# Kernel tuning notes

Hardware: AMD Instinct MI355X
Metric: run time of the kernel (lower is better)

The kernel has to match this reference:

```python
import jax, jax.numpy as jnp
import numpy as np

HEADS = 16
DIM_HEAD = 64
SCALE = 8.0
NUM_NULL_KV = 2
NON_CAUSAL_PREFIX = 64
LN_EPS = 1e-5

def _l2norm(t):
    # F.normalize: t / max(||t||_2, eps)
    n = jnp.sqrt(jnp.sum(t * t, axis=-1, keepdims=True))
    return t / jnp.maximum(n, 1e-12)

def _layer_norm(x, gamma):
    mu = jnp.mean(x, axis=-1, keepdims=True)
    var = jnp.mean((x - mu) ** 2, axis=-1, keepdims=True)
    return (x - mu) * jax.lax.rsqrt(var + LN_EPS) * gamma  # beta buffer is zeros

def setup_inputs() -> dict:
    key = jax.random.key(0)
    ks = jax.random.split(key, 6)
    b, n, dim = 2, 2048, 1024
    inner = HEADS * DIM_HEAD
    return {
        "x": jax.random.normal(ks[0], (b, n, dim), jnp.float32),
        "gamma": jnp.ones((dim,), jnp.float32),
        "Wq": jax.random.normal(ks[1], (dim, inner), jnp.float32) * (dim ** -0.5),
        "Wkv": jax.random.normal(ks[2], (dim, 2 * DIM_HEAD), jnp.float32) * (dim ** -0.5),
        "q_scale": jnp.ones((DIM_HEAD,), jnp.float32),
        "k_scale": jnp.ones((DIM_HEAD,), jnp.float32),
        "null_kv": jax.random.normal(ks[3], (2, NUM_NULL_KV, DIM_HEAD), jnp.float32),
        "Wout": jax.random.normal(ks[4], (inner, dim), jnp.float32) * (inner ** -0.5),
    }

def reference(x, gamma, Wq, Wkv, q_scale, k_scale, null_kv, Wout):
    b, n, dim = x.shape
    # NOTE: in the torch module, kv_input = x BEFORE self.norm is applied
    kv = jnp.einsum('bnd,de->bne', x, Wkv)          # [b, n, 2*dh]
    k, v = kv[..., :DIM_HEAD], kv[..., DIM_HEAD:]    # single shared kv head (MQA)
    xn = _layer_norm(x, gamma)
    q = jnp.einsum('bnd,de->bne', xn, Wq)            # [b, n, h*dh]
    # null kv prepended
    null_k = jnp.broadcast_to(null_kv[0], (b, NUM_NULL_KV, DIM_HEAD))
    null_v = jnp.broadcast_to(null_kv[1], (b, NUM_NULL_KV, DIM_HEAD))
    k = jnp.concatenate([null_k, k], axis=1)         # [b, j, dh]
    v = jnp.concatenate([null_v, v], axis=1)
    q = q.reshape(b, n, HEADS, DIM_HEAD).transpose(0, 2, 1, 3)  # [b, h, n, dh]
    q = _l2norm(q) * q_scale
    k = _l2norm(k) * k_scale
    sim = jnp.einsum('bhid,bjd->bhij', q, k) * SCALE  # [b, h, i, j]
    i, j = n, k.shape[1]
    rows = jnp.arange(i)[:, None]
    cols = jnp.arange(j)[None, :]
    causal_mask = cols > rows + (j - i)               # triu(j - i + 1)
    prefix_free = (rows < NON_CAUSAL_PREFIX) & (cols < NON_CAUSAL_PREFIX + (j - i))
    causal_mask = causal_mask & (~prefix_free)
    neg = -jnp.finfo(sim.dtype).max
    sim = jnp.where(causal_mask, neg, sim)
    attn = jax.nn.softmax(sim, axis=-1)
    out = jnp.einsum('bhij,bjd->bhid', attn, v)       # [b, h, n, dh]
    out = out.transpose(0, 2, 1, 3).reshape(b, n, HEADS * DIM_HEAD)
    return jnp.einsum('bne,ed->bnd', out, Wout)
```

## Files before the change

kernel.cpp:

```cpp
#include <hip/hip_runtime.h>

typedef _Float16 h16;
typedef _Float16 f16x8 __attribute__((ext_vector_type(8)));
typedef _Float16 f16x4 __attribute__((ext_vector_type(4)));
typedef float f32x4 __attribute__((ext_vector_type(4)));

#define KSCALE_FOLD 11.541560327111707f

__global__ __launch_bounds__(256) void pre_k(const float* __restrict__ Wq,
    const float* __restrict__ Wkv, const float* __restrict__ Wout,
    const float* __restrict__ gamma, const float* __restrict__ x,
    const float* __restrict__ nkv, const float* __restrict__ kscale,
    h16* __restrict__ W1t, h16* __restrict__ Wot, float* __restrict__ cq,
    float* __restrict__ mu, float* __restrict__ rr, h16* __restrict__ xh,
    h16* __restrict__ Kh, h16* __restrict__ Vth)
{
    __shared__ float ts[64][65];
    int pid = blockIdx.x;
    int tid = threadIdx.x;
    if (pid < 544) {
        int bx = pid & 15, by = pid >> 4;
        int c = tid & 63, rc = tid >> 6;
        const float* src; int ld, scol, drow0; h16* dst; bool useg = false;
        if (by < 16)      { src = Wq;   ld = 1024; scol = by*64;       dst = W1t; drow0 = scol;        useg = true; }
        else if (by < 18) { src = Wkv;  ld = 128;  scol = (by-16)*64;  dst = W1t; drow0 = 1024 + scol; }
        else              { src = Wout; ld = 1024; scol = (by-18)*64;  dst = Wot; drow0 = scol; }
        float part = 0.f;
#pragma unroll
        for (int i = 0; i < 16; ++i) {
            int r = rc*16 + i;
            float v = src[(size_t)(bx*64 + r)*ld + scol + c];
            if (useg) v *= gamma[bx*64 + r];
            part += v;
            ts[r][c] = v;
        }
        if (useg) atomicAdd(&cq[scol + c], part);
        __syncthreads();
#pragma unroll
        for (int i = 0; i < 16; ++i) {
            int r = rc*16 + i;
            dst[(size_t)(drow0 + r)*1024 + bx*64 + c] = (h16)ts[c][r];
        }
    } else if (pid < 1568) {
        int w = tid >> 6, l = tid & 63;
        int row = (pid - 544)*4 + w;
        const float* xr = x + (size_t)row*1024;
        float s = 0.f, ss = 0.f;
        float4 v[4];
#pragma unroll
        for (int i = 0; i < 4; ++i) {
            v[i] = *(const float4*)(xr + i*256 + l*4);
            s  += v[i].x + v[i].y + v[i].z + v[i].w;
            ss += v[i].x*v[i].x + v[i].y*v[i].y + v[i].z*v[i].z + v[i].w*v[i].w;
        }
#pragma unroll
        for (int m = 1; m < 64; m <<= 1) { s += __shfl_xor(s, m); ss += __shfl_xor(ss, m); }
        float m_ = s * (1.f/1024.f);
        float var = ss * (1.f/1024.f) - m_*m_;
        float r_ = rsqrtf(var + 1e-5f);
        if (l == 0) { mu[row] = m_; rr[row] = r_; }
        h16* xo = xh + (size_t)row*1024;
#pragma unroll
        for (int i = 0; i < 4; ++i) {
            f16x4 hv = { (h16)v[i].x, (h16)v[i].y, (h16)v[i].z, (h16)v[i].w };
            *(f16x4*)(xo + i*256 + l*4) = hv;
        }
    } else {
        int nb = pid - 1568;
        if (nb == 0 && tid < 128) {
            int t = tid >> 6, d = tid & 63;
            float kv = nkv[(0*2 + t)*64 + d];
            float ss = kv*kv;
#pragma unroll
            for (int m = 1; m < 64; m <<= 1) ss += __shfl_xor(ss, m);
            float inv = 1.f / fmaxf(sqrtf(ss), 1e-12f);
            h16 kvh = (h16)(kv * inv * kscale[d] * KSCALE_FOLD);
            Kh[(size_t)(0*2112 + t)*64 + d] = kvh;
            Kh[(size_t)(1*2112 + t)*64 + d] = kvh;
            float nv = nkv[(2 + t)*64 + d];
            Vth[(size_t)(0*64 + d)*2112 + t] = (h16)nv;
            Vth[(size_t)(1*64 + d)*2112 + t] = (h16)nv;
        }
        for (int idx = nb*256 + tid; idx < 2*62*64; idx += 2048) {
            int b = idx / (62*64), rem = idx % (62*64);
            int j = 2050 + rem/64, d = rem & 63;
            Kh[((size_t)b*2112 + j)*64 + d] = (h16)0.f;
            Vth[((size_t)b*64 + d)*2112 + j] = (h16)0.f;
        }
    }
}

template<int MODE>
__global__ __launch_bounds__(256) void gemm_k(
    const h16* __restrict__ A, const h16* __restrict__ B,
    const float* __restrict__ mu, const float* __restrict__ rr, const float* __restrict__ cq,
    const float* __restrict__ qscale, const float* __restrict__ kscale,
    h16* __restrict__ Qh, h16* __restrict__ Kh, h16* __restrict__ Vth, float* __restrict__ outp)
{
    __shared__ h16 As[2][128*64];
    __shared__ h16 Bs[2][64*64];
    int tid = threadIdx.x;
    int w = tid >> 6, l = tid & 63;
    int lq = l & 15, qq = l >> 4;
    int arow0 = blockIdx.y*128, bcol0 = blockIdx.x*64;
    const int K = 1024;
    f32x4 acc[2][4] = {};

    auto STAGE = [&](int buf, int kt) {
#pragma unroll
        for (int i = 0; i < 4; ++i) {
            int s = i*256 + tid;
            int row = s >> 3;
            int cb = ((s & 7)*16) ^ ((row & 7) << 4);
            const char* asrc = (const char*)(A + (size_t)(arow0 + row)*K + kt) + cb;
            __builtin_amdgcn_global_load_lds(
                (const __attribute__((address_space(1))) unsigned int*)asrc,
                (__attribute__((address_space(3))) unsigned int*)((char*)&As[buf][0] + s*16), 16, 0, 0);
        }
#pragma unroll
        for (int i = 0; i < 2; ++i) {
            int s = i*256 + tid;
            int row = s >> 3;
            int cb = ((s & 7)*16) ^ ((row & 7) << 4);
            const char* bsrc = (const char*)(B + (size_t)(bcol0 + row)*K + kt) + cb;
            __builtin_amdgcn_global_load_lds(
                (const __attribute__((address_space(1))) unsigned int*)bsrc,
                (__attribute__((address_space(3))) unsigned int*)((char*)&Bs[buf][0] + s*16), 16, 0, 0);
        }
    };

    STAGE(0, 0);
    int cur = 0;
    for (int kt = 0; kt < K; kt += 64) {
        int nkt = (kt + 64 < K) ? kt + 64 : kt;
        STAGE(cur ^ 1, nkt);
        asm volatile("s_waitcnt vmcnt(6)" ::: "memory");
        __builtin_amdgcn_s_barrier();
        __builtin_amdgcn_sched_barrier(0);
        const char* Ab = (const char*)&As[cur][0];
        const char* Bb = (const char*)&Bs[cur][0];
#pragma unroll
        for (int kc = 0; kc < 2; ++kc) {
            int cb = (kc*64 + qq*16) ^ ((lq & 7) << 4);
            f16x8 af[2], bf[4];
#pragma unroll
            for (int mt = 0; mt < 2; ++mt)
                af[mt] = *(const f16x8*)(Ab + (w*32 + mt*16 + lq)*128 + cb);
#pragma unroll
            for (int nt = 0; nt < 4; ++nt)
                bf[nt] = *(const f16x8*)(Bb + (nt*16 + lq)*128 + cb);
#pragma unroll
            for (int mt = 0; mt < 2; ++mt)
#pragma unroll
                for (int nt = 0; nt < 4; ++nt)
                    acc[mt][nt] = __builtin_amdgcn_mfma_f32_16x16x32_f16(af[mt], bf[nt], acc[mt][nt], 0, 0, 0);
        }
        __builtin_amdgcn_sched_barrier(0);
        __builtin_amdgcn_s_barrier();
        cur ^= 1;
    }
    asm volatile("s_waitcnt vmcnt(0)" ::: "memory");

    int wrow0 = arow0 + w*32;
    int bx = blockIdx.x;
    if (MODE == 1) {
#pragma unroll
        for (int mt = 0; mt < 2; ++mt)
#pragma unroll
            for (int nt = 0; nt < 4; ++nt)
#pragma unroll
                for (int i = 0; i < 4; ++i)
                    outp[(size_t)(wrow0 + mt*16 + qq*4 + i)*1024 + bcol0 + nt*16 + lq] = acc[mt][nt][i];
        return;
    }
    if (bx < 16) {
        float cqv[4], qs[4];
#pragma unroll
        for (int nt = 0; nt < 4; ++nt) {
            cqv[nt] = cq[bcol0 + nt*16 + lq];
            qs[nt] = qscale[nt*16 + lq];
        }
#pragma unroll
        for (int mt = 0; mt < 2; ++mt) {
            float muv[4], rv[4], ssq[4], qv[4][4];
#pragma unroll
            for (int i = 0; i < 4; ++i) {
                int row = wrow0 + mt*16 + qq*4 + i;
                muv[i] = mu[row]; rv[i] = rr[row]; ssq[i] = 0.f;
            }
#pragma unroll
            for (int nt = 0; nt < 4; ++nt)
#pragma unroll
                for (int i = 0; i < 4; ++i) {
                    float q = rv[i]*(acc[mt][nt][i] - muv[i]*cqv[nt]);
                    qv[nt][i] = q; ssq[i] += q*q;
                }
#pragma unroll
            for (int i = 0; i < 4; ++i) {
                float s2 = ssq[i];
                s2 += __shfl_xor(s2, 1); s2 += __shfl_xor(s2, 2);
                s2 += __shfl_xor(s2, 4); s2 += __shfl_xor(s2, 8);
                ssq[i] = 1.f / fmaxf(sqrtf(s2), 1e-12f);
            }
#pragma unroll
            for (int nt = 0; nt < 4; ++nt)
#pragma unroll
                for (int i = 0; i < 4; ++i) {
                    int row = wrow0 + mt*16 + qq*4 + i;
                    Qh[(size_t)row*1024 + bcol0 + nt*16 + lq] = (h16)(qv[nt][i]*ssq[i]*qs[nt]);
                }
        }
    } else if (bx == 16) {
        float ks[4];
#pragma unroll
        for (int nt = 0; nt < 4; ++nt) ks[nt] = kscale[nt*16 + lq] * KSCALE_FOLD;
#pragma unroll
        for (int mt = 0; mt < 2; ++mt) {
            float ssq[4] = {0.f, 0.f, 0.f, 0.f};
#pragma unroll
            for (int nt = 0; nt < 4; ++nt)
#pragma unroll
                for (int i = 0; i < 4; ++i) ssq[i] += acc[mt][nt][i]*acc[mt][nt][i];
#pragma unroll
            for (int i = 0; i < 4; ++i) {
                float s2 = ssq[i];
                s2 += __shfl_xor(s2, 1); s2 += __shfl_xor(s2, 2);
                s2 += __shfl_xor(s2, 4); s2 += __shfl_xor(s2, 8);
                ssq[i] = 1.f / fmaxf(sqrtf(s2), 1e-12f);
            }
#pragma unroll
            for (int nt = 0; nt < 4; ++nt)
#pragma unroll
                for (int i = 0; i < 4; ++i) {
                    int row = wrow0 + mt*16 + qq*4 + i;
                    int b = row >> 11, ii = row & 2047;
                    Kh[((size_t)b*2112 + 2 + ii)*64 + nt*16 + lq] = (h16)(acc[mt][nt][i]*ssq[i]*ks[nt]);
                }
        }
    } else {
#pragma unroll
        for (int mt = 0; mt < 2; ++mt)
#pragma unroll
            for (int nt = 0; nt < 4; ++nt)
#pragma unroll
                for (int i = 0; i < 4; ++i) {
                    int row = wrow0 + mt*16 + qq*4 + i;
                    int b = row >> 11, ii = row & 2047;
                    Vth[((size_t)b*64 + nt*16 + lq)*2112 + 2 + ii] = (h16)acc[mt][nt][i];
                }
    }
}

__global__ __launch_bounds__(512, 4) void attn_k(const h16* __restrict__ Qh,
    const h16* __restrict__ Kh, const h16* __restrict__ Vth, h16* __restrict__ Oh)
{
    __shared__ h16 KVs[2][2][64*64];
    __shared__ h16 Ps[8][16*64];
    int id = blockIdx.x;
    int hp = id & 7;
    int b = (id >> 3) & 1;
    int u = id >> 4;
    int qt = (u < 16) ? u : 47 - u;
    int tid = threadIdx.x, w = tid >> 6, l = tid & 63;
    int h = hp*2 + (w >> 2);
    int wq = w & 3;
    int lq = l & 15, qq = l >> 4;
    int qstart = qt * 64;
    int q0w = qstart + wq * 16;
    h16* P = &Ps[w][0];
    int xs = (lq & 7) << 4;

    f16x8 qf[2];
#pragma unroll
    for (int kc = 0; kc < 2; ++kc)
        qf[kc] = *(const f16x8*)(Qh + (size_t)(b*2048 + q0w + lq)*1024 + h*64 + kc*32 + qq*8);

    int qrow = q0w + lq;
    int thr = (qrow < 64) ? 65 : qrow + 2;

    int srow = tid >> 3;
    int cbs = ((tid & 7)*16) ^ ((srow & 7) << 4);
    const char* ksrc = (const char*)(Kh + (size_t)b*2112*64) + (size_t)srow*128 + cbs;
    const char* vsrc = (const char*)(Vth + (size_t)b*64*2112) + (size_t)srow*4224 + cbs;

    f32x4 oacc[4] = {};
    float lrun = 0.f;

    int lastc = qstart + 65;
    int ntile = lastc/64 + 1;

    auto STAGE = [&](int buf, int kv0) {
        __builtin_amdgcn_global_load_lds(
            (const __attribute__((address_space(1))) unsigned int*)(ksrc + (size_t)kv0*128),
            (__attribute__((address_space(3))) unsigned int*)((char*)&KVs[buf][0][0] + tid*16), 16, 0, 0);
        __builtin_amdgcn_global_load_lds(
            (const __attribute__((address_space(1))) unsigned int*)(vsrc + (size_t)kv0*2),
            (__attribute__((address_space(3))) unsigned int*)((char*)&KVs[buf][1][0] + tid*16), 16, 0, 0);
    };

    STAGE(0, 0);
    int cur = 0;
    for (int t = 0; t < ntile; ++t) {
        int kv0 = t*64;
        int nxt = (t + 1 < ntile) ? t + 1 : t;
        STAGE(cur ^ 1, nxt*64);
        asm volatile("s_waitcnt vmcnt(2)" ::: "memory");
        __builtin_amdgcn_s_barrier();
        __builtin_amdgcn_sched_barrier(0);

        bool active = (kv0 <= q0w + 17) || (q0w < 64 && kv0 < 66);
        if (active) {
            const char* Kl = (const char*)&KVs[cur][0][0];
            const char* Vl = (const char*)&KVs[cur][1][0];
            f32x4 s[4] = {};
#pragma unroll
            for (int kc = 0; kc < 2; ++kc) {
                int ko = (kc*64 + qq*16) ^ xs;
                f16x8 kf[4];
#pragma unroll
                for (int mt = 0; mt < 4; ++mt)
                    kf[mt] = *(const f16x8*)(Kl + (mt*16 + lq)*128 + ko);
#pragma unroll
                for (int mt = 0; mt < 4; ++mt)
                    s[mt] = __builtin_amdgcn_mfma_f32_16x16x32_f16(kf[mt], qf[kc], s[mt], 0, 0, 0);
            }
            if (kv0 + 63 > q0w + 2) {
#pragma unroll
                for (int mt = 0; mt < 4; ++mt)
#pragma unroll
                    for (int i = 0; i < 4; ++i) {
                        int kv = kv0 + mt*16 + qq*4 + i;
                        if (kv > thr) s[mt][i] = -__builtin_inff();
                    }
            }
            float ps = 0.f;
#pragma unroll
            for (int mt = 0; mt < 4; ++mt)
#pragma unroll
                for (int i = 0; i < 4; ++i) {
                    float p = exp2f(s[mt][i]);
                    s[mt][i] = p; ps += p;
                }
            ps += __shfl_xor(ps, 16);
            ps += __shfl_xor(ps, 32);
            lrun += ps;
#pragma unroll
            for (int mt = 0; mt < 4; ++mt) {
                uint2 pk;
                pk.x = __builtin_bit_cast(unsigned int, __builtin_amdgcn_cvt_pkrtz(s[mt][0], s[mt][1]));
                pk.y = __builtin_bit_cast(unsigned int, __builtin_amdgcn_cvt_pkrtz(s[mt][2], s[mt][3]));
                *(uint2*)((char*)P + lq*128 + ((mt*32 + qq*8) ^ xs)) = pk;
            }
#pragma unroll
            for (int kc = 0; kc < 2; ++kc) {
                int ko = (kc*64 + qq*16) ^ xs;
                f16x8 pf = *(const f16x8*)((const char*)P + lq*128 + ko);
#pragma unroll
                for (int dm = 0; dm < 4; ++dm) {
                    f16x8 vf = *(const f16x8*)(Vl + (dm*16 + lq)*128 + ko);
                    oacc[dm] = __builtin_amdgcn_mfma_f32_16x16x32_f16(vf, pf, oacc[dm], 0, 0, 0);
                }
            }
        }
        __builtin_amdgcn_sched_barrier(0);
        __builtin_amdgcn_s_barrier();
        cur ^= 1;
    }
    asm volatile("s_waitcnt vmcnt(0)" ::: "memory");

    float inv = 1.f / lrun;
#pragma unroll
    for (int dm = 0; dm < 4; ++dm) {
        f16x4 ov;
#pragma unroll
        for (int i = 0; i < 4; ++i) ov[i] = (h16)(oacc[dm][i]*inv);
        *(f16x4*)(Oh + (size_t)(b*2048 + q0w + lq)*1024 + h*64 + dm*16 + qq*4) = ov;
    }
}

extern "C" void kernel_launch(void* const* d_in, const int* in_sizes, int n_in,
                              void* d_out, int out_size, void* d_ws, size_t ws_size,
                              hipStream_t stream)
{
    const float* x      = (const float*)d_in[0];
    const float* gamma  = (const float*)d_in[1];
    const float* Wq     = (const float*)d_in[2];
    const float* Wkv    = (const float*)d_in[3];
    const float* qscale = (const float*)d_in[4];
    const float* kscale = (const float*)d_in[5];
    const float* nkv    = (const float*)d_in[6];
    const float* Wout   = (const float*)d_in[7];
    float* out = (float*)d_out;
    char* ws = (char*)d_ws;

    h16* xh   = (h16*)(ws);
    h16* Qh   = (h16*)(ws + 8388608);
    h16* Oh   = (h16*)(ws + 16777216);
    h16* W1t  = (h16*)(ws + 25165824);
    h16* Wot  = (h16*)(ws + 27525120);
    h16* Kh   = (h16*)(ws + 29622272);
    h16* Vth  = (h16*)(ws + 30162944);
    float* cq = (float*)(ws + 30703616);
    float* mu = (float*)(ws + 30707712);
    float* rr = (float*)(ws + 30724096);

    hipMemsetAsync(cq, 0, 4096, stream);
    pre_k<<<dim3(1576), 256, 0, stream>>>(Wq, Wkv, Wout, gamma, x, nkv, kscale,
                                          W1t, Wot, cq, mu, rr, xh, Kh, Vth);
    gemm_k<0><<<dim3(18, 32), 256, 0, stream>>>(xh, W1t, mu, rr, cq, qscale, kscale, Qh, Kh, Vth, out);
    attn_k<<<dim3(512), 512, 0, stream>>>(Qh, Kh, Vth, Oh);
    gemm_k<1><<<dim3(16, 32), 256, 0, stream>>>(Oh, Wot, mu, rr, cq, qscale, kscale, Qh, Kh, Vth, out);
}
```

Before: 102.3 us.

## Read K/V directly from global in attention, drop LDS staging and barriers

The attention kernel no longer stages K and V tiles into shared memory with async global-to-LDS loads and double buffering. Each wave now loads its K and V fragments straight from global memory, relying on the caches because K and V are shared across heads (MQA). Blocks shrink to 4 waves handling one head, the grid doubles, and each wave runs only its own causal tile count, so block-wide barriers go away. The cost is more global and cache traffic per wave and no explicit prefetch to hide load latency.

```diff
diff --git a/kernel.cpp b/kernel.cpp
--- a/kernel.cpp
+++ b/kernel.cpp
@@ -251,25 +251,25 @@
     }
 }
 
-__global__ __launch_bounds__(512, 4) void attn_k(const h16* __restrict__ Qh,
+__global__ __launch_bounds__(256) void attn_k(const h16* __restrict__ Qh,
     const h16* __restrict__ Kh, const h16* __restrict__ Vth, h16* __restrict__ Oh)
 {
-    __shared__ h16 KVs[2][2][64*64];
-    __shared__ h16 Ps[8][16*64];
+    __shared__ h16 Ps[4][16*64];
     int id = blockIdx.x;
-    int hp = id & 7;
-    int b = (id >> 3) & 1;
-    int u = id >> 4;
+    int h = id & 15;
+    int b = (id >> 4) & 1;
+    int u = id >> 5;
     int qt = (u < 16) ? u : 47 - u;
     int tid = threadIdx.x, w = tid >> 6, l = tid & 63;
-    int h = hp*2 + (w >> 2);
-    int wq = w & 3;
     int lq = l & 15, qq = l >> 4;
     int qstart = qt * 64;
-    int q0w = qstart + wq * 16;
+    int q0w = qstart + w * 16;
     h16* P = &Ps[w][0];
     int xs = (lq & 7) << 4;
 
+    const h16* Kb = Kh + (size_t)b*2112*64;
+    const h16* Vb = Vth + (size_t)b*64*2112;
+
     f16x8 qf[2];
 #pragma unroll
     for (int kc = 0; kc < 2; ++kc)
@@ -278,95 +278,64 @@
     int qrow = q0w + lq;
     int thr = (qrow < 64) ? 65 : qrow + 2;
 
-    int srow = tid >> 3;
-    int cbs = ((tid & 7)*16) ^ ((srow & 7) << 4);
-    const char* ksrc = (const char*)(Kh + (size_t)b*2112*64) + (size_t)srow*128 + cbs;
-    const char* vsrc = (const char*)(Vth + (size_t)b*64*2112) + (size_t)srow*4224 + cbs;
+    int lastkv = (q0w < 64) ? 65 : q0w + 17;
+    int ntile = lastkv/64 + 1;
 
     f32x4 oacc[4] = {};
     float lrun = 0.f;
 
-    int lastc = qstart + 65;
-    int ntile = lastc/64 + 1;
-
-    auto STAGE = [&](int buf, int kv0) {
-        __builtin_amdgcn_global_load_lds(
-            (const __attribute__((address_space(1))) unsigned int*)(ksrc + (size_t)kv0*128),
-            (__attribute__((address_space(3))) unsigned int*)((char*)&KVs[buf][0][0] + tid*16), 16, 0, 0);
-        __builtin_amdgcn_global_load_lds(
-            (const __attribute__((address_space(1))) unsigned int*)(vsrc + (size_t)kv0*2),
-            (__attribute__((address_space(3))) unsigned int*)((char*)&KVs[buf][1][0] + tid*16), 16, 0, 0);
-    };
-
-    STAGE(0, 0);
-    int cur = 0;
     for (int t = 0; t < ntile; ++t) {
         int kv0 = t*64;
-        int nxt = (t + 1 < ntile) ? t + 1 : t;
-        STAGE(cur ^ 1, nxt*64);
-        asm volatile("s_waitcnt vmcnt(2)" ::: "memory");
-        __builtin_amdgcn_s_barrier();
-        __builtin_amdgcn_sched_barrier(0);
-
-        bool active = (kv0 <= q0w + 17) || (q0w < 64 && kv0 < 66);
-        if (active) {
-            const char* Kl = (const char*)&KVs[cur][0][0];
-            const char* Vl = (const char*)&KVs[cur][1][0];
-            f32x4 s[4] = {};
-#pragma unroll
-            for (int kc = 0; kc < 2; ++kc) {
-                int ko = (kc*64 + qq*16) ^ xs;
-                f16x8 kf[4];
-#pragma unroll
-                for (int mt = 0; mt < 4; ++mt)
-                    kf[mt] = *(const f16x8*)(Kl + (mt*16 + lq)*128 + ko);
-#pragma unroll
-                for (int mt = 0; mt < 4; ++mt)
-                    s[mt] = __builtin_amdgcn_mfma_f32_16x16x32_f16(kf[mt], qf[kc], s[mt], 0, 0, 0);
-            }
-            if (kv0 + 63 > q0w + 2) {
-#pragma unroll
-                for (int mt = 0; mt < 4; ++mt)
-#pragma unroll
-                    for (int i = 0; i < 4; ++i) {
-                        int kv = kv0 + mt*16 + qq*4 + i;
-                        if (kv > thr) s[mt][i] = -__builtin_inff();
-                    }
-            }
-            float ps = 0.f;
+        f32x4 s[4] = {};
+#pragma unroll
+        for (int kc = 0; kc < 2; ++kc) {
+            const h16* Kp = Kb + (size_t)kv0*64 + kc*32 + qq*8;
+            f16x8 kf[4];
 #pragma unroll
             for (int mt = 0; mt < 4; ++mt)
-#pragma unroll
-                for (int i = 0; i < 4; ++i) {
-                    float p = exp2f(s[mt][i]);
-                    s[mt][i] = p; ps += p;
-                }
-            ps += __shfl_xor(ps, 16);
-            ps += __shfl_xor(ps, 32);
-            lrun += ps;
-#pragma unroll
-            for (int mt = 0; mt < 4; ++mt) {
-                uint2 pk;
-                pk.x = __builtin_bit_cast(unsigned int, __builtin_amdgcn_cvt_pkrtz(s[mt][0], s[mt][1]));
-                pk.y = __builtin_bit_cast(unsigned int, __builtin_amdgcn_cvt_pkrtz(s[mt][2], s[mt][3]));
-                *(uint2*)((char*)P + lq*128 + ((mt*32 + qq*8) ^ xs)) = pk;
-            }
-#pragma unroll
-            for (int kc = 0; kc < 2; ++kc) {
-                int ko = (kc*64 + qq*16) ^ xs;
-                f16x8 pf = *(const f16x8*)((const char*)P + lq*128 + ko);
-#pragma unroll
-                for (int dm = 0; dm < 4; ++dm) {
-                    f16x8 vf = *(const f16x8*)(Vl + (dm*16 + lq)*128 + ko);
-                    oacc[dm] = __builtin_amdgcn_mfma_f32_16x16x32_f16(vf, pf, oacc[dm], 0, 0, 0);
-                }
-            }
-        }
-        __builtin_amdgcn_sched_barrier(0);
-        __builtin_amdgcn_s_barrier();
-        cur ^= 1;
-    }
-    asm volatile("s_waitcnt vmcnt(0)" ::: "memory");
+                kf[mt] = *(const f16x8*)(Kp + (mt*16 + lq)*64);
+#pragma unroll
+            for (int mt = 0; mt < 4; ++mt)
+                s[mt] = __builtin_amdgcn_mfma_f32_16x16x32_f16(kf[mt], qf[kc], s[mt], 0, 0, 0);
+        }
+        if (kv0 + 63 > q0w + 2) {
+#pragma unroll
+            for (int mt = 0; mt < 4; ++mt)
+#pragma unroll
+                for (int i = 0; i < 4; ++i) {
+                    int kv = kv0 + mt*16 + qq*4 + i;
+                    if (kv > thr) s[mt][i] = -__builtin_inff();
+                }
+        }
+        float ps = 0.f;
+#pragma unroll
+        for (int mt = 0; mt < 4; ++mt)
+#pragma unroll
+            for (int i = 0; i < 4; ++i) {
+                float p = exp2f(s[mt][i]);
+                s[mt][i] = p; ps += p;
+            }
+        ps += __shfl_xor(ps, 16);
+        ps += __shfl_xor(ps, 32);
+        lrun += ps;
+#pragma unroll
+        for (int mt = 0; mt < 4; ++mt) {
+            uint2 pk;
+            pk.x = __builtin_bit_cast(unsigned int, __builtin_amdgcn_cvt_pkrtz(s[mt][0], s[mt][1]));
+            pk.y = __builtin_bit_cast(unsigned int, __builtin_amdgcn_cvt_pkrtz(s[mt][2], s[mt][3]));
+            *(uint2*)((char*)P + lq*128 + ((mt*32 + qq*8) ^ xs)) = pk;
+        }
+#pragma unroll
+        for (int kc = 0; kc < 2; ++kc) {
+            f16x8 pf = *(const f16x8*)((const char*)P + lq*128 + ((kc*64 + qq*16) ^ xs));
+            const h16* Vp = Vb + kv0 + kc*32 + qq*8;
+#pragma unroll
+            for (int dm = 0; dm < 4; ++dm) {
+                f16x8 vf = *(const f16x8*)(Vp + (size_t)(dm*16 + lq)*2112);
+                oacc[dm] = __builtin_amdgcn_mfma_f32_16x16x32_f16(vf, pf, oacc[dm], 0, 0, 0);
+            }
+        }
+    }
 
     float inv = 1.f / lrun;
 #pragma unroll
@@ -408,6 +377,6 @@
     pre_k<<<dim3(1576), 256, 0, stream>>>(Wq, Wkv, Wout, gamma, x, nkv, kscale,
                                           W1t, Wot, cq, mu, rr, xh, Kh, Vth);
     gemm_k<0><<<dim3(18, 32), 256, 0, stream>>>(xh, W1t, mu, rr, cq, qscale, kscale, Qh, Kh, Vth, out);
-    attn_k<<<dim3(512), 512, 0, stream>>>(Qh, Kh, Vth, Oh);
+    attn_k<<<dim3(1024), 256, 0, stream>>>(Qh, Kh, Vth, Oh);
     gemm_k<1><<<dim3(16, 32), 256, 0, stream>>>(Oh, Wot, mu, rr, cq, qscale, kscale, Qh, Kh, Vth, out);
 }
```

Result: slower. 206.5 us (+101.9%).

## Split attention blocks to one head each and compute row sums via MFMA

Applied to the files above, without the earlier changes.

The attention kernel now launches 1024 blocks of 256 threads, one (batch, head, q-tile) per block, instead of 512 blocks of 512 threads covering two heads. Each thread issues four global-to-LDS loads per stage to fill the K/V tile, and the vmcnt wait is adjusted to match. The softmax denominator is now accumulated with an extra MFMA against a vector of ones rather than with per-lane sums and cross-lane shuffles. exp2f is replaced by the raw hardware exp2 instruction. K/V tiles are now staged once per head rather than shared across two heads, which adds memory traffic in exchange for smaller blocks and better occupancy and balance.

```diff
diff --git a/kernel.cpp b/kernel.cpp
--- a/kernel.cpp
+++ b/kernel.cpp
@@ -6,6 +6,14 @@
 typedef float f32x4 __attribute__((ext_vector_type(4)));
 
 #define KSCALE_FOLD 11.541560327111707f
+
+#if __has_builtin(__builtin_amdgcn_exp2f)
+#define EXP2(x) __builtin_amdgcn_exp2f(x)
+#else
+static __device__ __forceinline__ float EXP2(float x) {
+    float r; asm("v_exp_f32 %0, %1" : "=v"(r) : "v"(x)); return r;
+}
+#endif
 
 __global__ __launch_bounds__(256) void pre_k(const float* __restrict__ Wq,
     const float* __restrict__ Wkv, const float* __restrict__ Wout,
@@ -251,22 +259,20 @@
     }
 }
 
-__global__ __launch_bounds__(512, 4) void attn_k(const h16* __restrict__ Qh,
+__global__ __launch_bounds__(256, 4) void attn_k(const h16* __restrict__ Qh,
     const h16* __restrict__ Kh, const h16* __restrict__ Vth, h16* __restrict__ Oh)
 {
     __shared__ h16 KVs[2][2][64*64];
-    __shared__ h16 Ps[8][16*64];
+    __shared__ h16 Ps[4][16*64];
     int id = blockIdx.x;
-    int hp = id & 7;
-    int b = (id >> 3) & 1;
-    int u = id >> 4;
+    int u = id >> 5;
     int qt = (u < 16) ? u : 47 - u;
+    int bh = id & 31;
+    int b = bh >> 4, h = bh & 15;
     int tid = threadIdx.x, w = tid >> 6, l = tid & 63;
-    int h = hp*2 + (w >> 2);
-    int wq = w & 3;
     int lq = l & 15, qq = l >> 4;
     int qstart = qt * 64;
-    int q0w = qstart + wq * 16;
+    int q0w = qstart + w * 16;
     h16* P = &Ps[w][0];
     int xs = (lq & 7) << 4;
 
@@ -275,27 +281,35 @@
     for (int kc = 0; kc < 2; ++kc)
         qf[kc] = *(const f16x8*)(Qh + (size_t)(b*2048 + q0w + lq)*1024 + h*64 + kc*32 + qq*8);
 
+    f16x8 ones;
+#pragma unroll
+    for (int i = 0; i < 8; ++i) ones[i] = (h16)1.f;
+
     int qrow = q0w + lq;
     int thr = (qrow < 64) ? 65 : qrow + 2;
 
-    int srow = tid >> 3;
-    int cbs = ((tid & 7)*16) ^ ((srow & 7) << 4);
-    const char* ksrc = (const char*)(Kh + (size_t)b*2112*64) + (size_t)srow*128 + cbs;
-    const char* vsrc = (const char*)(Vth + (size_t)b*64*2112) + (size_t)srow*4224 + cbs;
+    int cbs = ((tid & 7)*16) ^ (((tid >> 3) & 7) << 4);
+    const char* ksrc = (const char*)(Kh + (size_t)b*2112*64) + (size_t)(tid >> 3)*128 + cbs;
+    const char* vsrc = (const char*)(Vth + (size_t)b*64*2112) + (size_t)(tid >> 3)*4224 + cbs;
 
     f32x4 oacc[4] = {};
-    float lrun = 0.f;
+    f32x4 sacc = {};
 
     int lastc = qstart + 65;
+    if (lastc > 2049) lastc = 2049;
     int ntile = lastc/64 + 1;
 
     auto STAGE = [&](int buf, int kv0) {
-        __builtin_amdgcn_global_load_lds(
-            (const __attribute__((address_space(1))) unsigned int*)(ksrc + (size_t)kv0*128),
-            (__attribute__((address_space(3))) unsigned int*)((char*)&KVs[buf][0][0] + tid*16), 16, 0, 0);
-        __builtin_amdgcn_global_load_lds(
-            (const __attribute__((address_space(1))) unsigned int*)(vsrc + (size_t)kv0*2),
-            (__attribute__((address_space(3))) unsigned int*)((char*)&KVs[buf][1][0] + tid*16), 16, 0, 0);
+        const char* ks = ksrc + (size_t)kv0 * 128;
+        const char* vs = vsrc + (size_t)kv0 * 2;
+        __builtin_amdgcn_global_load_lds((const __attribute__((address_space(1))) unsigned int*)ks,
+            (__attribute__((address_space(3))) unsigned int*)(&KVs[buf][0][(w*8)*64]), 16, 0, 0);
+        __builtin_amdgcn_global_load_lds((const __attribute__((address_space(1))) unsigned int*)(ks + 32*128),
+            (__attribute__((address_space(3))) unsigned int*)(&KVs[buf][0][(32 + w*8)*64]), 16, 0, 0);
+        __builtin_amdgcn_global_load_lds((const __attribute__((address_space(1))) unsigned int*)vs,
+            (__attribute__((address_space(3))) unsigned int*)(&KVs[buf][1][(w*8)*64]), 16, 0, 0);
+        __builtin_amdgcn_global_load_lds((const __attribute__((address_space(1))) unsigned int*)(vs + (size_t)32*4224),
+            (__attribute__((address_space(3))) unsigned int*)(&KVs[buf][1][(32 + w*8)*64]), 16, 0, 0);
     };
 
     STAGE(0, 0);
@@ -304,7 +318,7 @@
         int kv0 = t*64;
         int nxt = (t + 1 < ntile) ? t + 1 : t;
         STAGE(cur ^ 1, nxt*64);
-        asm volatile("s_waitcnt vmcnt(2)" ::: "memory");
+        asm volatile("s_waitcnt vmcnt(4)" ::: "memory");
         __builtin_amdgcn_s_barrier();
         __builtin_amdgcn_sched_barrier(0);
 
@@ -333,17 +347,11 @@
                         if (kv > thr) s[mt][i] = -__builtin_inff();
                     }
             }
-            float ps = 0.f;
 #pragma unroll
             for (int mt = 0; mt < 4; ++mt)
 #pragma unroll
-                for (int i = 0; i < 4; ++i) {
-                    float p = exp2f(s[mt][i]);
-                    s[mt][i] = p; ps += p;
-                }
-            ps += __shfl_xor(ps, 16);
-            ps += __shfl_xor(ps, 32);
-            lrun += ps;
+                for (int i = 0; i < 4; ++i)
+                    s[mt][i] = EXP2(s[mt][i]);
 #pragma unroll
             for (int mt = 0; mt < 4; ++mt) {
                 uint2 pk;
@@ -360,6 +368,7 @@
                     f16x8 vf = *(const f16x8*)(Vl + (dm*16 + lq)*128 + ko);
                     oacc[dm] = __builtin_amdgcn_mfma_f32_16x16x32_f16(vf, pf, oacc[dm], 0, 0, 0);
                 }
+                sacc = __builtin_amdgcn_mfma_f32_16x16x32_f16(ones, pf, sacc, 0, 0, 0);
             }
         }
         __builtin_amdgcn_sched_barrier(0);
@@ -368,7 +377,7 @@
     }
     asm volatile("s_waitcnt vmcnt(0)" ::: "memory");
 
-    float inv = 1.f / lrun;
+    float inv = 1.f / sacc[0];
 #pragma unroll
     for (int dm = 0; dm < 4; ++dm) {
         f16x4 ov;
@@ -408,6 +417,6 @@
     pre_k<<<dim3(1576), 256, 0, stream>>>(Wq, Wkv, Wout, gamma, x, nkv, kscale,
                                           W1t, Wot, cq, mu, rr, xh, Kh, Vth);
     gemm_k<0><<<dim3(18, 32), 256, 0, stream>>>(xh, W1t, mu, rr, cq, qscale, kscale, Qh, Kh, Vth, out);
-    attn_k<<<dim3(512), 512, 0, stream>>>(Qh, Kh, Vth, Oh);
+    attn_k<<<dim3(1024), 256, 0, stream>>>(Qh, Kh, Vth, Oh);
     gemm_k<1><<<dim3(16, 32), 256, 0, stream>>>(Oh, Wot, mu, rr, cq, qscale, kscale, Qh, Kh, Vth, out);
 }
```

Result: faster. 89.93 us (-12.1%).
